# Kernel tuning notes

Hardware: AMD Instinct MI355X
Metric: run time of the kernel (lower is better)

Reference implementation:

```python
import jax, jax.numpy as jnp
import numpy as np

B, C_IN, C_OUT, H, W, K = 8, 64, 64, 64, 64, 9
T = H * W  # 4096 tokens
EPS = 1e-12  # F.normalize eps


def setup_inputs() -> dict:
    key = jax.random.key(0)
    ks = jax.random.split(key, 7)
    x = jax.random.normal(ks[0], (B, C_IN, H, W), dtype=jnp.float32)
    Wq = jax.random.normal(ks[1], (T, T), dtype=jnp.float32) * 0.02
    Wk = jax.random.normal(ks[2], (T, T), dtype=jnp.float32) * 0.02
    Wv = jax.random.normal(ks[3], (T, T), dtype=jnp.float32) * 0.02
    Wo = jax.random.normal(ks[4], (T, T), dtype=jnp.float32) * 0.02
    conv_w = jax.random.normal(ks[5], (C_OUT, C_IN, K), dtype=jnp.float32) * 0.05
    conv_b = jax.random.normal(ks[6], (C_OUT,), dtype=jnp.float32) * 0.01
    return {"x": x, "Wq": Wq, "Wk": Wk, "Wv": Wv, "Wo": Wo,
            "conv_w": conv_w, "conv_b": conv_b}


def reference(x, Wq, Wk, Wv, Wo, conv_w, conv_b):
    Bq, Cc, Hh, Ww = x.shape
    Tt = Hh * Ww
    xf = x.reshape(Bq, Cc, Tt)  # flatten(start_dim=2)
    # nn.Linear over the token (last) dim: y[...,s] = sum_t x[...,t] * W[s,t]
    q = jnp.einsum('bct,st->bcs', xf, Wq)
    k = jnp.einsum('bct,st->bcs', xf, Wk)
    v = jnp.einsum('bct,st->bcs', xf, Wv)
    # cosine similarity over channel dim (dim=1), clamp to >= 0
    kn = k / jnp.maximum(jnp.linalg.norm(k, axis=1, keepdims=True), EPS)
    qn = q / jnp.maximum(jnp.linalg.norm(q, axis=1, keepdims=True), EPS)
    sim = jnp.clip(jnp.einsum('bct,bcs->bts', kn, qn), 0.0, None)  # [B,T,T]
    # top-K most similar neighbors per token (largest=True for similarity)
    _, idx = jax.lax.top_k(sim, K)  # [B,T,K] int32
    # gather neighbor values: prime[b,c,t,j] = v[b,c,idx[b,t,j]]
    gather = jax.vmap(lambda vv, ii: vv[:, ii])  # vv:[C,T], ii:[T,K] -> [C,T,K]
    prime = gather(v, idx).reshape(Bq, Cc, Tt * K)
    # Conv1d(kernel=K, stride=K, padding=0): aggregates each K-neighbor group
    out = jax.lax.conv_general_dilated(
        prime, conv_w, window_strides=(K,), padding='VALID',
        dimension_numbers=('NCH', 'OIH', 'NCH'))  # [B,C_OUT,T]
    out = out + conv_b[None, :, None]
    out = jnp.einsum('bct,st->bcs', out, Wo)  # w_o over token dim
    return out.reshape(Bq, conv_w.shape[0], Hh, Ww)
```

## Files before the change

kernel.cpp:

```cpp
#include <hip/hip_runtime.h>

#define T4096 4096
#define CH 64
typedef unsigned long long u64;

__global__ __launch_bounds__(512) void gemm_qkv(
    const float* __restrict__ X,
    const float* __restrict__ Wq, const float* __restrict__ Wk, const float* __restrict__ Wv,
    float* __restrict__ QT, float* __restrict__ KT, float* __restrict__ VT)
{
    const float* W = (blockIdx.z == 0) ? Wq : (blockIdx.z == 1) ? Wk : Wv;
    float*       O = (blockIdx.z == 0) ? QT : (blockIdx.z == 1) ? KT : VT;
    const int b  = blockIdx.y;
    const int s0 = blockIdx.x * 128;

    __shared__ float As[64][132];
    __shared__ float Bs[64][68];

    const int tid = threadIdx.x;
    const int tx = tid & 15;   const int c0 = tx * 4;
    const int my = tid >> 4;   const int m0 = my * 4;
    const int lr = tid >> 3;
    const int lk = (tid & 7) * 4;
    const int sw = lk;

    float acc[4][4];
#pragma unroll
    for (int i = 0; i < 4; ++i)
#pragma unroll
        for (int j = 0; j < 4; ++j) acc[i][j] = 0.f;

    const float* Xb = X + (size_t)b * CH * T4096;

    for (int k0 = 0; k0 < T4096; k0 += 64) {
#pragma unroll
        for (int kk = 0; kk < 2; ++kk) {
            const int kb = 32 * kk + lk;
#pragma unroll
            for (int p = 0; p < 2; ++p) {
                int row = lr + 64 * p;
                float4 v = *(const float4*)(W + (size_t)(s0 + row) * T4096 + k0 + kb);
                int col = row ^ sw;
                As[kb + 0][col] = v.x; As[kb + 1][col] = v.y;
                As[kb + 2][col] = v.z; As[kb + 3][col] = v.w;
            }
            {
                int row = lr;
                float4 v = *(const float4*)(Xb + (size_t)row * T4096 + k0 + kb);
                int col = row ^ sw;
                Bs[kb + 0][col] = v.x; Bs[kb + 1][col] = v.y;
                Bs[kb + 2][col] = v.z; Bs[kb + 3][col] = v.w;
            }
        }
        __syncthreads();
#pragma unroll
        for (int k = 0; k < 64; ++k) {
            const int swk = k & 28;
            float4 a  = *(const float4*)&As[k][m0 ^ swk];
            float4 bv = *(const float4*)&Bs[k][c0 ^ swk];
            float am[4] = {a.x, a.y, a.z, a.w};
            float bn[4] = {bv.x, bv.y, bv.z, bv.w};
#pragma unroll
            for (int i = 0; i < 4; ++i)
#pragma unroll
                for (int j = 0; j < 4; ++j) acc[i][j] = fmaf(am[i], bn[j], acc[i][j]);
        }
        __syncthreads();
    }
    if (blockIdx.z == 0) {
#pragma unroll
        for (int i = 0; i < 4; ++i) {
            int s = s0 + m0 + i;
            *(float4*)(O + ((((size_t)b * 64 + (s >> 6)) * 16 + tx) * 64 + (s & 63)) * 4) =
                make_float4(acc[i][0], acc[i][1], acc[i][2], acc[i][3]);
        }
    } else {
#pragma unroll
        for (int i = 0; i < 4; ++i) {
            *(float4*)(O + ((size_t)b * T4096 + s0 + m0 + i) * CH + c0) =
                make_float4(acc[i][0], acc[i][1], acc[i][2], acc[i][3]);
        }
    }
}

__global__ __launch_bounds__(256) void normalize_qk(float* __restrict__ QT, float* __restrict__ KT)
{
    int gtok = blockIdx.x * 4 + (threadIdx.x >> 6);
    int lane = threadIdx.x & 63;
    bool isQ = (gtok < 8 * T4096);
    int t = gtok & (T4096 - 1);
    int b = (gtok >> 12) & 7;
    float* p;
    if (isQ) p = QT + ((((size_t)b * 64 + (t >> 6)) * 16 + (lane >> 2)) * 64 + (t & 63)) * 4 + (lane & 3);
    else     p = KT + ((size_t)b * T4096 + t) * CH + lane;
    float v = *p;
    float ss = v * v;
#pragma unroll
    for (int off = 32; off; off >>= 1) ss += __shfl_xor(ss, off);
    float n = fmaxf(sqrtf(ss), 1e-12f);
    *p = v / n;
}

__global__ __launch_bounds__(512) void sim_topk(
    const float* __restrict__ Qr, const float* __restrict__ KT, int* __restrict__ IDX)
{
    const int wg = blockIdx.x;
    const int b  = wg & 7;
    const int t0 = (wg >> 3) * 32;

    __shared__ float Kn[32][68];

    const int tid = threadIdx.x;
    const int tx = tid & 31;
    const int ty = tid >> 5;

    {
        int row = tid >> 4; int cc = (tid & 15) * 4;
        *(float4*)&Kn[row][cc] =
            *(const float4*)(KT + ((size_t)b * T4096 + t0 + row) * CH + cc);
    }
    __syncthreads();

    u64 tv[2][9];
#pragma unroll
    for (int r = 0; r < 2; ++r)
#pragma unroll
        for (int q = 0; q < 9; ++q) tv[r][q] = 0ULL;
    u64 thr[2] = {0ULL, 0ULL};
    unsigned thr_hi[2] = {0u, 0u};

    const float* qb0 = Qr + ((size_t)b * 64 * 1024 + tx) * 4;

    for (int it = 0; it < 16; ++it) {
        const float* bp = qb0 + (size_t)(it * 4) * 4096;
        float acc[2][8];
#pragma unroll
        for (int c = 0; c < 8; ++c) { acc[0][c] = 0.f; acc[1][c] = 0.f; }

#pragma unroll 1
        for (int c4g = 0; c4g < 16; ++c4g) {
            float4 qv[8];
#pragma unroll
            for (int cc = 0; cc < 8; ++cc)
                qv[cc] = *(const float4*)(bp + (size_t)(cc >> 1) * 4096
                                             + c4g * 256 + (cc & 1) * 128);
            float4 k0 = *(const float4*)&Kn[ty][c4g * 4];
            float4 k1 = *(const float4*)&Kn[16 + ty][c4g * 4];
#pragma unroll
            for (int cc = 0; cc < 8; ++cc) {
                acc[0][cc] = fmaf(k0.x, qv[cc].x, acc[0][cc]);
                acc[0][cc] = fmaf(k0.y, qv[cc].y, acc[0][cc]);
                acc[0][cc] = fmaf(k0.z, qv[cc].z, acc[0][cc]);
                acc[0][cc] = fmaf(k0.w, qv[cc].w, acc[0][cc]);
                acc[1][cc] = fmaf(k1.x, qv[cc].x, acc[1][cc]);
                acc[1][cc] = fmaf(k1.y, qv[cc].y, acc[1][cc]);
                acc[1][cc] = fmaf(k1.z, qv[cc].z, acc[1][cc]);
                acc[1][cc] = fmaf(k1.w, qv[cc].w, acc[1][cc]);
            }
        }

        bool ins = false;
        const int sb = it * 256 + tx;
#pragma unroll
        for (int rr = 0; rr < 2; ++rr)
#pragma unroll
            for (int cc = 0; cc < 8; ++cc) {
                float v = fmaxf(acc[rr][cc], 0.f);
                unsigned vb = __float_as_uint(v);
                if (vb >= thr_hi[rr]) {
                    int s = sb + 32 * cc;
                    u64 key = ((u64)vb << 32) | (u64)(4095 - s);
                    if (key > thr[rr]) {
                        u64 cv = key;
#pragma unroll
                        for (int p = 0; p < 9; ++p) {
                            u64 t  = tv[rr][p];
                            bool g = cv > t;
                            tv[rr][p] = g ? cv : t;
                            cv        = g ? t  : cv;
                        }
                        ins = true;
                    }
                }
            }
        if (__any(ins)) {
#pragma unroll
            for (int r = 0; r < 2; ++r) {
                u64 m = tv[r][8];
#pragma unroll
                for (int msk = 1; msk < 32; msk <<= 1) {
                    u64 o = __shfl_xor(m, msk);
                    if (o > m) m = o;
                }
                thr[r] = m;
                thr_hi[r] = (unsigned)(m >> 32);
            }
        }
    }

#pragma unroll
    for (int rr = 0; rr < 2; ++rr) {
        u64 mv[9];
#pragma unroll
        for (int q = 0; q < 9; ++q) mv[q] = tv[rr][q];
        const int outrow = t0 + rr * 16 + ty;
        int* dst = IDX + ((size_t)b * T4096 + outrow) * 9;
        for (int sel = 0; sel < 9; ++sel) {
            u64 bk = mv[0]; int bl = tx;
#pragma unroll
            for (int m = 1; m < 32; m <<= 1) {
                u64 ok = __shfl_xor(bk, m);
                int ol = __shfl_xor(bl, m);
                if (ok > bk) { bk = ok; bl = ol; }
            }
            if (tx == 0) dst[sel] = 4095 - (int)(unsigned)bk;
            if (tx == bl) {
#pragma unroll
                for (int q = 0; q < 8; ++q) mv[q] = mv[q + 1];
                mv[8] = 0ULL;
            }
        }
    }
}

__global__ void transpose_w(const float* __restrict__ cw, float* __restrict__ wT3)
{
    int idx = blockIdx.x * 256 + threadIdx.x;
    if (idx >= 64 * 64 * 9) return;
    int q   = idx & 3;
    int o   = (idx >> 2) & 63;
    int i4g = (idx >> 8) & 15;
    int j   = idx >> 12;
    wT3[idx] = cw[o * 576 + (i4g * 4 + q) * 9 + j];
}

__global__ __launch_bounds__(256) void gather_conv(
    const float* __restrict__ VT, const int* __restrict__ IDX,
    const float* __restrict__ wT3, const float* __restrict__ conv_b,
    float* __restrict__ out1)
{
    const int b  = blockIdx.y;
    const int w  = threadIdx.x >> 6;
    const int o  = threadIdx.x & 63;
    const int t0 = (blockIdx.x * 4 + w) * 4;

    __shared__ float vv[4][4][9][64];
    __shared__ int   nb[4][36];

    if (o < 36) nb[w][o] = IDX[((size_t)b * T4096 + t0) * 9 + o];
    __syncthreads();

#pragma unroll
    for (int tok = 0; tok < 4; ++tok)
#pragma unroll
        for (int j = 0; j < 9; ++j) {
            int n = nb[w][tok * 9 + j];
            vv[w][tok][j][o] = VT[((size_t)b * T4096 + n) * CH + o];
        }
    __syncthreads();

    float cb = conv_b[o];
    float a0 = cb, a1 = cb, a2 = cb, a3 = cb;
    for (int j = 0; j < 9; ++j) {
#pragma unroll
        for (int i4 = 0; i4 < 16; ++i4) {
            float4 w4 = *(const float4*)(wT3 + (((size_t)j * 16 + i4) * 64 + o) * 4);
            float4 v0 = *(const float4*)&vv[w][0][j][i4 * 4];
            float4 v1 = *(const float4*)&vv[w][1][j][i4 * 4];
            float4 v2 = *(const float4*)&vv[w][2][j][i4 * 4];
            float4 v3 = *(const float4*)&vv[w][3][j][i4 * 4];
            a0 = fmaf(v0.x, w4.x, a0); a0 = fmaf(v0.y, w4.y, a0); a0 = fmaf(v0.z, w4.z, a0); a0 = fmaf(v0.w, w4.w, a0);
            a1 = fmaf(v1.x, w4.x, a1); a1 = fmaf(v1.y, w4.y, a1); a1 = fmaf(v1.z, w4.z, a1); a1 = fmaf(v1.w, w4.w, a1);
            a2 = fmaf(v2.x, w4.x, a2); a2 = fmaf(v2.y, w4.y, a2); a2 = fmaf(v2.z, w4.z, a2); a2 = fmaf(v2.w, w4.w, a2);
            a3 = fmaf(v3.x, w4.x, a3); a3 = fmaf(v3.y, w4.y, a3); a3 = fmaf(v3.z, w4.z, a3); a3 = fmaf(v3.w, w4.w, a3);
        }
    }
    out1[((size_t)b * T4096 + t0 + 0) * CH + o] = a0;
    out1[((size_t)b * T4096 + t0 + 1) * CH + o] = a1;
    out1[((size_t)b * T4096 + t0 + 2) * CH + o] = a2;
    out1[((size_t)b * T4096 + t0 + 3) * CH + o] = a3;
}

__global__ __launch_bounds__(256) void gemm_out(
    const float* __restrict__ out1, const float* __restrict__ Wo, float* __restrict__ Out)
{
    const int b  = blockIdx.y;
    const int s0 = blockIdx.x * 64;
    __shared__ float As[64][68];
    __shared__ float Bs[64][68];
    const int tid = threadIdx.x;
    const int tx = tid & 15;  const int sl = tx * 4;
    const int my = tid >> 4;  const int c0 = my * 4;
    const int lk = (tid & 7) * 4;
    const int sw = lk;

    float acc[4][4];
#pragma unroll
    for (int i = 0; i < 4; ++i)
#pragma unroll
        for (int j = 0; j < 4; ++j) acc[i][j] = 0.f;

    for (int k0 = 0; k0 < T4096; k0 += 64) {
        {
            int r  = tid >> 2;
            int cL = (tid & 3) * 16;
            const float* src = out1 + ((size_t)b * T4096 + k0 + r) * CH + cL;
#pragma unroll
            for (int q = 0; q < 4; ++q)
                *(float4*)&As[r][cL + 4 * q] = *(const float4*)(src + 4 * q);
        }
#pragma unroll
        for (int kk = 0; kk < 2; ++kk) {
            const int kb = 32 * kk + lk;
#pragma unroll
            for (int p = 0; p < 2; ++p) {
                int row = (tid >> 3) + 32 * p;
                float4 v = *(const float4*)(Wo + (size_t)(s0 + row) * T4096 + k0 + kb);
                int col = row ^ sw;
                Bs[kb + 0][col] = v.x; Bs[kb + 1][col] = v.y;
                Bs[kb + 2][col] = v.z; Bs[kb + 3][col] = v.w;
            }
        }
        __syncthreads();
#pragma unroll
        for (int k = 0; k < 64; ++k) {
            const int swk = k & 28;
            float4 a  = *(const float4*)&As[k][c0];
            float4 bv = *(const float4*)&Bs[k][sl ^ swk];
            float av[4] = {a.x, a.y, a.z, a.w};
            float bn[4] = {bv.x, bv.y, bv.z, bv.w};
#pragma unroll
            for (int i = 0; i < 4; ++i)
#pragma unroll
                for (int j = 0; j < 4; ++j) acc[i][j] = fmaf(av[i], bn[j], acc[i][j]);
        }
        __syncthreads();
    }
#pragma unroll
    for (int i = 0; i < 4; ++i) {
        float* dst = Out + ((size_t)b * CH + c0 + i) * T4096 + s0 + sl;
        *(float4*)dst = make_float4(acc[i][0], acc[i][1], acc[i][2], acc[i][3]);
    }
}

extern "C" void kernel_launch(void* const* d_in, const int* in_sizes, int n_in,
                              void* d_out, int out_size, void* d_ws, size_t ws_size,
                              hipStream_t stream)
{
    const float* x  = (const float*)d_in[0];
    const float* Wq = (const float*)d_in[1];
    const float* Wk = (const float*)d_in[2];
    const float* Wv = (const float*)d_in[3];
    const float* Wo = (const float*)d_in[4];
    const float* cw = (const float*)d_in[5];
    const float* cb = (const float*)d_in[6];
    float* Out = (float*)d_out;

    char* ws = (char*)d_ws;
    float* QT   = (float*)(ws);
    float* KT   = (float*)(ws + (size_t)8  * 1024 * 1024);
    float* VT   = (float*)(ws + (size_t)16 * 1024 * 1024);
    int*   IDXb = (int*)  (ws + (size_t)24 * 1024 * 1024);
    float* wT3  = (float*)(ws + (size_t)26 * 1024 * 1024);
    float* out1 = QT;

    gemm_qkv<<<dim3(32, 8, 3), dim3(512), 0, stream>>>(x, Wq, Wk, Wv, QT, KT, VT);
    normalize_qk<<<dim3(16384), dim3(256), 0, stream>>>(QT, KT);
    sim_topk<<<dim3(1024), dim3(512), 0, stream>>>(QT, KT, IDXb);
    transpose_w<<<dim3(144), dim3(256), 0, stream>>>(cw, wT3);
    gather_conv<<<dim3(256, 8), dim3(256), 0, stream>>>(VT, IDXb, wT3, cb, out1);
    gemm_out<<<dim3(64, 8), dim3(256), 0, stream>>>(out1, Wo, Out);
}
```

Before: 1.618 ms.

## Restructure sim_topk to one row per thread with split-S partial top-k merge

```diff
diff --git a/kernel.cpp b/kernel.cpp
--- a/kernel.cpp
+++ b/kernel.cpp
@@ -67,19 +67,10 @@
         }
         __syncthreads();
     }
-    if (blockIdx.z == 0) {
-#pragma unroll
-        for (int i = 0; i < 4; ++i) {
-            int s = s0 + m0 + i;
-            *(float4*)(O + ((((size_t)b * 64 + (s >> 6)) * 16 + tx) * 64 + (s & 63)) * 4) =
-                make_float4(acc[i][0], acc[i][1], acc[i][2], acc[i][3]);
-        }
-    } else {
-#pragma unroll
-        for (int i = 0; i < 4; ++i) {
-            *(float4*)(O + ((size_t)b * T4096 + s0 + m0 + i) * CH + c0) =
-                make_float4(acc[i][0], acc[i][1], acc[i][2], acc[i][3]);
-        }
+#pragma unroll
+    for (int i = 0; i < 4; ++i) {
+        *(float4*)(O + ((size_t)b * T4096 + s0 + m0 + i) * CH + c0) =
+            make_float4(acc[i][0], acc[i][1], acc[i][2], acc[i][3]);
     }
 }
 
@@ -87,12 +78,9 @@
 {
     int gtok = blockIdx.x * 4 + (threadIdx.x >> 6);
     int lane = threadIdx.x & 63;
-    bool isQ = (gtok < 8 * T4096);
-    int t = gtok & (T4096 - 1);
-    int b = (gtok >> 12) & 7;
-    float* p;
-    if (isQ) p = QT + ((((size_t)b * 64 + (t >> 6)) * 16 + (lane >> 2)) * 64 + (t & 63)) * 4 + (lane & 3);
-    else     p = KT + ((size_t)b * T4096 + t) * CH + lane;
+    float* base = (gtok < 8 * T4096) ? QT : KT;
+    int t = gtok & (8 * T4096 - 1);
+    float* p = base + (size_t)t * CH + lane;
     float v = *p;
     float ss = v * v;
 #pragma unroll
@@ -101,126 +89,111 @@
     *p = v / n;
 }
 
-__global__ __launch_bounds__(512) void sim_topk(
-    const float* __restrict__ Qr, const float* __restrict__ KT, int* __restrict__ IDX)
+__global__ __launch_bounds__(256, 2) void sim_topk(
+    const float* __restrict__ QT, const float* __restrict__ KT,
+    unsigned* __restrict__ PKv, unsigned short* __restrict__ PKi)
 {
     const int wg = blockIdx.x;
     const int b  = wg & 7;
-    const int t0 = (wg >> 3) * 32;
-
-    __shared__ float Kn[32][68];
-
-    const int tid = threadIdx.x;
-    const int tx = tid & 31;
-    const int ty = tid >> 5;
-
-    {
-        int row = tid >> 4; int cc = (tid & 15) * 4;
-        *(float4*)&Kn[row][cc] =
-            *(const float4*)(KT + ((size_t)b * T4096 + t0 + row) * CH + cc);
-    }
-    __syncthreads();
-
-    u64 tv[2][9];
-#pragma unroll
-    for (int r = 0; r < 2; ++r)
-#pragma unroll
-        for (int q = 0; q < 9; ++q) tv[r][q] = 0ULL;
-    u64 thr[2] = {0ULL, 0ULL};
-    unsigned thr_hi[2] = {0u, 0u};
-
-    const float* qb0 = Qr + ((size_t)b * 64 * 1024 + tx) * 4;
-
-    for (int it = 0; it < 16; ++it) {
-        const float* bp = qb0 + (size_t)(it * 4) * 4096;
-        float acc[2][8];
-#pragma unroll
-        for (int c = 0; c < 8; ++c) { acc[0][c] = 0.f; acc[1][c] = 0.f; }
+    const int sp = (wg >> 3) & 3;
+    const int rt = wg >> 5;
+    const int row = rt * 256 + threadIdx.x;
+
+    float4 kr[16];
+    const float* kp = KT + ((size_t)b * T4096 + row) * CH;
+#pragma unroll
+    for (int i = 0; i < 16; ++i) kr[i] = *(const float4*)(kp + 4 * i);
+
+    u64 tv[9];
+#pragma unroll
+    for (int q = 0; q < 9; ++q) tv[q] = 0ULL;
+    unsigned thr_hi = 0u;
+
+    const float* qb = QT + ((size_t)b * T4096 + sp * 1024) * CH;
 
 #pragma unroll 1
-        for (int c4g = 0; c4g < 16; ++c4g) {
-            float4 qv[8];
-#pragma unroll
-            for (int cc = 0; cc < 8; ++cc)
-                qv[cc] = *(const float4*)(bp + (size_t)(cc >> 1) * 4096
-                                             + c4g * 256 + (cc & 1) * 128);
-            float4 k0 = *(const float4*)&Kn[ty][c4g * 4];
-            float4 k1 = *(const float4*)&Kn[16 + ty][c4g * 4];
-#pragma unroll
-            for (int cc = 0; cc < 8; ++cc) {
-                acc[0][cc] = fmaf(k0.x, qv[cc].x, acc[0][cc]);
-                acc[0][cc] = fmaf(k0.y, qv[cc].y, acc[0][cc]);
-                acc[0][cc] = fmaf(k0.z, qv[cc].z, acc[0][cc]);
-                acc[0][cc] = fmaf(k0.w, qv[cc].w, acc[0][cc]);
-                acc[1][cc] = fmaf(k1.x, qv[cc].x, acc[1][cc]);
-                acc[1][cc] = fmaf(k1.y, qv[cc].y, acc[1][cc]);
-                acc[1][cc] = fmaf(k1.z, qv[cc].z, acc[1][cc]);
-                acc[1][cc] = fmaf(k1.w, qv[cc].w, acc[1][cc]);
-            }
-        }
-
-        bool ins = false;
-        const int sb = it * 256 + tx;
-#pragma unroll
-        for (int rr = 0; rr < 2; ++rr)
-#pragma unroll
-            for (int cc = 0; cc < 8; ++cc) {
-                float v = fmaxf(acc[rr][cc], 0.f);
-                unsigned vb = __float_as_uint(v);
-                if (vb >= thr_hi[rr]) {
-                    int s = sb + 32 * cc;
-                    u64 key = ((u64)vb << 32) | (u64)(4095 - s);
-                    if (key > thr[rr]) {
-                        u64 cv = key;
-#pragma unroll
-                        for (int p = 0; p < 9; ++p) {
-                            u64 t  = tv[rr][p];
-                            bool g = cv > t;
-                            tv[rr][p] = g ? cv : t;
-                            cv        = g ? t  : cv;
-                        }
-                        ins = true;
+    for (int qs = 0; qs < 256; ++qs) {
+        const float* base = qb + (size_t)qs * (4 * CH);
+        float a0 = 0.f, a1 = 0.f, a2 = 0.f, a3 = 0.f;
+#pragma unroll
+        for (int c = 0; c < 16; ++c) {
+            float4 q0 = *(const float4*)(base + c * 4);
+            float4 q1 = *(const float4*)(base + CH + c * 4);
+            float4 q2 = *(const float4*)(base + 2 * CH + c * 4);
+            float4 q3 = *(const float4*)(base + 3 * CH + c * 4);
+            a0 = fmaf(kr[c].x, q0.x, a0); a0 = fmaf(kr[c].y, q0.y, a0);
+            a0 = fmaf(kr[c].z, q0.z, a0); a0 = fmaf(kr[c].w, q0.w, a0);
+            a1 = fmaf(kr[c].x, q1.x, a1); a1 = fmaf(kr[c].y, q1.y, a1);
+            a1 = fmaf(kr[c].z, q1.z, a1); a1 = fmaf(kr[c].w, q1.w, a1);
+            a2 = fmaf(kr[c].x, q2.x, a2); a2 = fmaf(kr[c].y, q2.y, a2);
+            a2 = fmaf(kr[c].z, q2.z, a2); a2 = fmaf(kr[c].w, q2.w, a2);
+            a3 = fmaf(kr[c].x, q3.x, a3); a3 = fmaf(kr[c].y, q3.y, a3);
+            a3 = fmaf(kr[c].z, q3.z, a3); a3 = fmaf(kr[c].w, q3.w, a3);
+        }
+        const int s0 = sp * 1024 + qs * 4;
+        float av[4] = {a0, a1, a2, a3};
+#pragma unroll
+        for (int j = 0; j < 4; ++j) {
+            float v = fmaxf(av[j], 0.f);
+            unsigned vb = __float_as_uint(v);
+            if (vb >= thr_hi) {
+                u64 key = ((u64)vb << 32) | (u64)(4095 - (s0 + j));
+                if (key > tv[8]) {
+                    u64 cv = key;
+#pragma unroll
+                    for (int p = 0; p < 9; ++p) {
+                        u64 t  = tv[p];
+                        bool g = cv > t;
+                        tv[p] = g ? cv : t;
+                        cv    = g ? t  : cv;
                     }
+                    thr_hi = (unsigned)(tv[8] >> 32);
                 }
             }
-        if (__any(ins)) {
-#pragma unroll
-            for (int r = 0; r < 2; ++r) {
-                u64 m = tv[r][8];
-#pragma unroll
-                for (int msk = 1; msk < 32; msk <<= 1) {
-                    u64 o = __shfl_xor(m, msk);
-                    if (o > m) m = o;
-                }
-                thr[r] = m;
-                thr_hi[r] = (unsigned)(m >> 32);
-            }
-        }
-    }
-
-#pragma unroll
-    for (int rr = 0; rr < 2; ++rr) {
-        u64 mv[9];
-#pragma unroll
-        for (int q = 0; q < 9; ++q) mv[q] = tv[rr][q];
-        const int outrow = t0 + rr * 16 + ty;
-        int* dst = IDX + ((size_t)b * T4096 + outrow) * 9;
-        for (int sel = 0; sel < 9; ++sel) {
-            u64 bk = mv[0]; int bl = tx;
-#pragma unroll
-            for (int m = 1; m < 32; m <<= 1) {
-                u64 ok = __shfl_xor(bk, m);
-                int ol = __shfl_xor(bl, m);
-                if (ok > bk) { bk = ok; bl = ol; }
-            }
-            if (tx == 0) dst[sel] = 4095 - (int)(unsigned)bk;
-            if (tx == bl) {
-#pragma unroll
-                for (int q = 0; q < 8; ++q) mv[q] = mv[q + 1];
-                mv[8] = 0ULL;
-            }
-        }
-    }
+        }
+    }
+
+    const size_t o = (((size_t)b * 4 + sp) * T4096 + row) * 9;
+#pragma unroll
+    for (int q = 0; q < 9; ++q) {
+        PKv[o + q] = (unsigned)(tv[q] >> 32);
+        PKi[o + q] = (unsigned short)(tv[q] & 0xffffULL);
+    }
+}
+
+__global__ __launch_bounds__(256) void topk_merge(
+    const unsigned* __restrict__ PKv, const unsigned short* __restrict__ PKi,
+    int* __restrict__ IDX)
+{
+    const int t = blockIdx.x * 256 + threadIdx.x;
+    const int b = t >> 12;
+    const int row = t & 4095;
+
+    u64 tv[9];
+#pragma unroll
+    for (int q = 0; q < 9; ++q) tv[q] = 0ULL;
+
+    for (int sp = 0; sp < 4; ++sp) {
+        const size_t o = (((size_t)b * 4 + sp) * T4096 + row) * 9;
+#pragma unroll 1
+        for (int q = 0; q < 9; ++q) {
+            u64 key = ((u64)PKv[o + q] << 32) | (u64)PKi[o + q];
+            if (key <= tv[8]) break;
+            u64 cv = key;
+#pragma unroll
+            for (int p = 0; p < 9; ++p) {
+                u64 tt = tv[p];
+                bool g = cv > tt;
+                tv[p] = g ? cv : tt;
+                cv    = g ? tt : cv;
+            }
+        }
+    }
+
+    int* dst = IDX + ((size_t)b * T4096 + row) * 9;
+#pragma unroll
+    for (int q = 0; q < 9; ++q)
+        dst[q] = 4095 - (int)(unsigned)(tv[q] & 0xffffULL);
 }
 
 __global__ void transpose_w(const float* __restrict__ cw, float* __restrict__ wT3)
@@ -364,9 +337,13 @@
     float* wT3  = (float*)(ws + (size_t)26 * 1024 * 1024);
     float* out1 = QT;
 
+    unsigned*       PKv = (unsigned*)d_out;
+    unsigned short* PKi = (unsigned short*)((char*)d_out + (size_t)5 * 1024 * 1024);
+
     gemm_qkv<<<dim3(32, 8, 3), dim3(512), 0, stream>>>(x, Wq, Wk, Wv, QT, KT, VT);
     normalize_qk<<<dim3(16384), dim3(256), 0, stream>>>(QT, KT);
-    sim_topk<<<dim3(1024), dim3(512), 0, stream>>>(QT, KT, IDXb);
+    sim_topk<<<dim3(512), dim3(256), 0, stream>>>(QT, KT, PKv, PKi);
+    topk_merge<<<dim3(128), dim3(256), 0, stream>>>(PKv, PKi, IDXb);
     transpose_w<<<dim3(144), dim3(256), 0, stream>>>(cw, wT3);
     gather_conv<<<dim3(256, 8), dim3(256), 0, stream>>>(VT, IDXb, wT3, cb, out1);
     gemm_out<<<dim3(64, 8), dim3(256), 0, stream>>>(out1, Wo, Out);
```

Result: slower. 1.870 ms (+15.6%).

## Stage Q tiles in shared memory and use 4x4 register tiling in sim_topk

Applied to the files above, without the earlier changes.

```diff
diff --git a/kernel.cpp b/kernel.cpp
--- a/kernel.cpp
+++ b/kernel.cpp
@@ -101,83 +101,100 @@
     *p = v / n;
 }
 
-__global__ __launch_bounds__(512) void sim_topk(
+__global__ __launch_bounds__(512, 2) void sim_topk(
     const float* __restrict__ Qr, const float* __restrict__ KT, int* __restrict__ IDX)
 {
     const int wg = blockIdx.x;
     const int b  = wg & 7;
-    const int t0 = (wg >> 3) * 32;
-
-    __shared__ float Kn[32][68];
-
-    const int tid = threadIdx.x;
-    const int tx = tid & 31;
-    const int ty = tid >> 5;
+    const int r0 = (wg >> 3) * 64;
+
+    __shared__ float Kn[64][68];
+    __shared__ float Qs[64][132];
+
+    const int tid  = threadIdx.x;
+    const int colg = tid & 31;
+    const int rowg = tid >> 5;
 
     {
-        int row = tid >> 4; int cc = (tid & 15) * 4;
-        *(float4*)&Kn[row][cc] =
-            *(const float4*)(KT + ((size_t)b * T4096 + t0 + row) * CH + cc);
-    }
-    __syncthreads();
-
-    u64 tv[2][9];
-#pragma unroll
-    for (int r = 0; r < 2; ++r)
+        int row = tid >> 3;
+        int c8  = (tid & 7) * 8;
+        const float* src = KT + ((size_t)b * T4096 + r0 + row) * CH + c8;
+        float4 v0 = *(const float4*)(src);
+        float4 v1 = *(const float4*)(src + 4);
+        int rp = row ^ ((tid & 7) << 3);
+        Kn[c8 + 0][rp] = v0.x; Kn[c8 + 1][rp] = v0.y;
+        Kn[c8 + 2][rp] = v0.z; Kn[c8 + 3][rp] = v0.w;
+        Kn[c8 + 4][rp] = v1.x; Kn[c8 + 5][rp] = v1.y;
+        Kn[c8 + 6][rp] = v1.z; Kn[c8 + 7][rp] = v1.w;
+    }
+
+    u64 tv[4][9];
+#pragma unroll
+    for (int r = 0; r < 4; ++r)
 #pragma unroll
         for (int q = 0; q < 9; ++q) tv[r][q] = 0ULL;
-    u64 thr[2] = {0ULL, 0ULL};
-    unsigned thr_hi[2] = {0u, 0u};
-
-    const float* qb0 = Qr + ((size_t)b * 64 * 1024 + tx) * 4;
-
-    for (int it = 0; it < 16; ++it) {
-        const float* bp = qb0 + (size_t)(it * 4) * 4096;
-        float acc[2][8];
-#pragma unroll
-        for (int c = 0; c < 8; ++c) { acc[0][c] = 0.f; acc[1][c] = 0.f; }
-
-#pragma unroll 1
-        for (int c4g = 0; c4g < 16; ++c4g) {
-            float4 qv[8];
-#pragma unroll
-            for (int cc = 0; cc < 8; ++cc)
-                qv[cc] = *(const float4*)(bp + (size_t)(cc >> 1) * 4096
-                                             + c4g * 256 + (cc & 1) * 128);
-            float4 k0 = *(const float4*)&Kn[ty][c4g * 4];
-            float4 k1 = *(const float4*)&Kn[16 + ty][c4g * 4];
-#pragma unroll
-            for (int cc = 0; cc < 8; ++cc) {
-                acc[0][cc] = fmaf(k0.x, qv[cc].x, acc[0][cc]);
-                acc[0][cc] = fmaf(k0.y, qv[cc].y, acc[0][cc]);
-                acc[0][cc] = fmaf(k0.z, qv[cc].z, acc[0][cc]);
-                acc[0][cc] = fmaf(k0.w, qv[cc].w, acc[0][cc]);
-                acc[1][cc] = fmaf(k1.x, qv[cc].x, acc[1][cc]);
-                acc[1][cc] = fmaf(k1.y, qv[cc].y, acc[1][cc]);
-                acc[1][cc] = fmaf(k1.z, qv[cc].z, acc[1][cc]);
-                acc[1][cc] = fmaf(k1.w, qv[cc].w, acc[1][cc]);
-            }
+    u64 thr[4] = {0ULL, 0ULL, 0ULL, 0ULL};
+    unsigned thr_hi[4] = {0u, 0u, 0u, 0u};
+
+    for (int chk = 0; chk < 32; ++chk) {
+        const int c0 = chk * 128;
+        __syncthreads();
+        {
+            int col  = tid >> 2;
+            int cQ   = (tid & 3) * 16;
+            int gcol = c0 + col;
+            const float* qb = Qr + ((((size_t)b * 64 + (gcol >> 6)) * 16 + (cQ >> 2)) * 64
+                                    + (gcol & 63)) * 4;
+            int cp = col ^ ((cQ >> 4) << 3);
+#pragma unroll
+            for (int i = 0; i < 4; ++i) {
+                float4 v = *(const float4*)(qb + (size_t)i * 256);
+                int c = cQ + i * 4;
+                Qs[c + 0][cp] = v.x; Qs[c + 1][cp] = v.y;
+                Qs[c + 2][cp] = v.z; Qs[c + 3][cp] = v.w;
+            }
+        }
+        __syncthreads();
+
+        float acc[4][4];
+#pragma unroll
+        for (int i = 0; i < 4; ++i)
+#pragma unroll
+            for (int j = 0; j < 4; ++j) acc[i][j] = 0.f;
+
+#pragma unroll 8
+        for (int c = 0; c < 64; ++c) {
+            const int g8 = ((c >> 3) & 7) << 3;
+            const int g4 = ((c >> 4) & 3) << 3;
+            float4 kv = *(const float4*)&Kn[c][(rowg * 4) ^ g8];
+            float4 qv = *(const float4*)&Qs[c][(colg * 4) ^ g4];
+            float km[4] = {kv.x, kv.y, kv.z, kv.w};
+            float qm[4] = {qv.x, qv.y, qv.z, qv.w};
+#pragma unroll
+            for (int i = 0; i < 4; ++i)
+#pragma unroll
+                for (int j = 0; j < 4; ++j)
+                    acc[i][j] = fmaf(km[i], qm[j], acc[i][j]);
         }
 
         bool ins = false;
-        const int sb = it * 256 + tx;
-#pragma unroll
-        for (int rr = 0; rr < 2; ++rr)
-#pragma unroll
-            for (int cc = 0; cc < 8; ++cc) {
-                float v = fmaxf(acc[rr][cc], 0.f);
+#pragma unroll
+        for (int i = 0; i < 4; ++i)
+#pragma unroll
+            for (int j = 0; j < 4; ++j) {
+                float v = fmaxf(acc[i][j], 0.f);
                 unsigned vb = __float_as_uint(v);
-                if (vb >= thr_hi[rr]) {
-                    int s = sb + 32 * cc;
+                if (vb >= thr_hi[i]) {
+                    int s = c0 + colg * 4 + j;
                     u64 key = ((u64)vb << 32) | (u64)(4095 - s);
-                    if (key > thr[rr]) {
+                    if (key > thr[i]) {
                         u64 cv = key;
 #pragma unroll
                         for (int p = 0; p < 9; ++p) {
-                            u64 t  = tv[rr][p];
+                            u64 t  = tv[i][p];
                             bool g = cv > t;
-                            tv[rr][p] = g ? cv : t;
-                            cv        = g ? t  : cv;
+                            tv[i][p] = g ? cv : t;
+                            cv       = g ? t  : cv;
                         }
                         ins = true;
                     }
@@ -185,7 +202,7 @@
             }
         if (__any(ins)) {
 #pragma unroll
-            for (int r = 0; r < 2; ++r) {
+            for (int r = 0; r < 4; ++r) {
                 u64 m = tv[r][8];
 #pragma unroll
                 for (int msk = 1; msk < 32; msk <<= 1) {
@@ -199,22 +216,22 @@
     }
 
 #pragma unroll
-    for (int rr = 0; rr < 2; ++rr) {
+    for (int i = 0; i < 4; ++i) {
         u64 mv[9];
 #pragma unroll
-        for (int q = 0; q < 9; ++q) mv[q] = tv[rr][q];
-        const int outrow = t0 + rr * 16 + ty;
+        for (int q = 0; q < 9; ++q) mv[q] = tv[i][q];
+        const int outrow = r0 + rowg * 4 + i;
         int* dst = IDX + ((size_t)b * T4096 + outrow) * 9;
         for (int sel = 0; sel < 9; ++sel) {
-            u64 bk = mv[0]; int bl = tx;
+            u64 bk = mv[0]; int bl = colg;
 #pragma unroll
             for (int m = 1; m < 32; m <<= 1) {
                 u64 ok = __shfl_xor(bk, m);
                 int ol = __shfl_xor(bl, m);
                 if (ok > bk) { bk = ok; bl = ol; }
             }
-            if (tx == 0) dst[sel] = 4095 - (int)(unsigned)bk;
-            if (tx == bl) {
+            if (colg == 0) dst[sel] = 4095 - (int)(unsigned)(bk & 0xffffULL);
+            if (colg == bl) {
 #pragma unroll
                 for (int q = 0; q < 8; ++q) mv[q] = mv[q + 1];
                 mv[8] = 0ULL;
@@ -366,7 +383,7 @@
 
     gemm_qkv<<<dim3(32, 8, 3), dim3(512), 0, stream>>>(x, Wq, Wk, Wv, QT, KT, VT);
     normalize_qk<<<dim3(16384), dim3(256), 0, stream>>>(QT, KT);
-    sim_topk<<<dim3(1024), dim3(512), 0, stream>>>(QT, KT, IDXb);
+    sim_topk<<<dim3(512), dim3(512), 0, stream>>>(QT, KT, IDXb);
     transpose_w<<<dim3(144), dim3(256), 0, stream>>>(cw, wT3);
     gather_conv<<<dim3(256, 8), dim3(256), 0, stream>>>(VT, IDXb, wT3, cb, out1);
     gemm_out<<<dim3(64, 8), dim3(256), 0, stream>>>(out1, Wo, Out);
```

Result: slower. 1.703 ms (+5.3%).

## Fuse Q/K normalization into QKV GEMM epilogue and enlarge per-thread tiles

Applied to the files above, without the earlier changes.

```diff
diff --git a/kernel.cpp b/kernel.cpp
--- a/kernel.cpp
+++ b/kernel.cpp
@@ -3,14 +3,14 @@
 #define T4096 4096
 #define CH 64
 typedef unsigned long long u64;
-
-__global__ __launch_bounds__(512) void gemm_qkv(
+typedef float v2f __attribute__((ext_vector_type(2)));
+
+__global__ __launch_bounds__(128) void gemm_qkv(
     const float* __restrict__ X,
     const float* __restrict__ Wq, const float* __restrict__ Wk, const float* __restrict__ Wv,
     float* __restrict__ QT, float* __restrict__ KT, float* __restrict__ VT)
 {
     const float* W = (blockIdx.z == 0) ? Wq : (blockIdx.z == 1) ? Wk : Wv;
-    float*       O = (blockIdx.z == 0) ? QT : (blockIdx.z == 1) ? KT : VT;
     const int b  = blockIdx.y;
     const int s0 = blockIdx.x * 128;
 
@@ -18,87 +18,100 @@
     __shared__ float Bs[64][68];
 
     const int tid = threadIdx.x;
-    const int tx = tid & 15;   const int c0 = tx * 4;
-    const int my = tid >> 4;   const int m0 = my * 4;
-    const int lr = tid >> 3;
-    const int lk = (tid & 7) * 4;
-    const int sw = lk;
-
-    float acc[4][4];
-#pragma unroll
-    for (int i = 0; i < 4; ++i)
-#pragma unroll
-        for (int j = 0; j < 4; ++j) acc[i][j] = 0.f;
+    const int txc = tid & 7;   const int c0 = txc * 8;
+    const int tym = tid >> 3;  const int m0 = tym * 8;
+    const int lk  = (tid & 15) * 4;
+    const int rA  = tid >> 4;
+    const int sw  = lk & 28;
+
+    float acc[8][8];
+#pragma unroll
+    for (int i = 0; i < 8; ++i)
+#pragma unroll
+        for (int j = 0; j < 8; ++j) acc[i][j] = 0.f;
 
     const float* Xb = X + (size_t)b * CH * T4096;
 
     for (int k0 = 0; k0 < T4096; k0 += 64) {
-#pragma unroll
-        for (int kk = 0; kk < 2; ++kk) {
-            const int kb = 32 * kk + lk;
-#pragma unroll
-            for (int p = 0; p < 2; ++p) {
-                int row = lr + 64 * p;
-                float4 v = *(const float4*)(W + (size_t)(s0 + row) * T4096 + k0 + kb);
-                int col = row ^ sw;
-                As[kb + 0][col] = v.x; As[kb + 1][col] = v.y;
-                As[kb + 2][col] = v.z; As[kb + 3][col] = v.w;
-            }
-            {
-                int row = lr;
-                float4 v = *(const float4*)(Xb + (size_t)row * T4096 + k0 + kb);
-                int col = row ^ sw;
-                Bs[kb + 0][col] = v.x; Bs[kb + 1][col] = v.y;
-                Bs[kb + 2][col] = v.z; Bs[kb + 3][col] = v.w;
-            }
+#pragma unroll 4
+        for (int p = 0; p < 16; ++p) {
+            int row = rA + 8 * p;
+            float4 v = *(const float4*)(W + (size_t)(s0 + row) * T4096 + k0 + lk);
+            int col = row ^ sw;
+            As[lk + 0][col] = v.x; As[lk + 1][col] = v.y;
+            As[lk + 2][col] = v.z; As[lk + 3][col] = v.w;
+        }
+#pragma unroll 4
+        for (int p = 0; p < 8; ++p) {
+            int row = rA + 8 * p;
+            float4 v = *(const float4*)(Xb + (size_t)row * T4096 + k0 + lk);
+            int col = row ^ sw;
+            Bs[lk + 0][col] = v.x; Bs[lk + 1][col] = v.y;
+            Bs[lk + 2][col] = v.z; Bs[lk + 3][col] = v.w;
         }
         __syncthreads();
 #pragma unroll
         for (int k = 0; k < 64; ++k) {
             const int swk = k & 28;
-            float4 a  = *(const float4*)&As[k][m0 ^ swk];
-            float4 bv = *(const float4*)&Bs[k][c0 ^ swk];
-            float am[4] = {a.x, a.y, a.z, a.w};
-            float bn[4] = {bv.x, bv.y, bv.z, bv.w};
-#pragma unroll
-            for (int i = 0; i < 4; ++i)
-#pragma unroll
-                for (int j = 0; j < 4; ++j) acc[i][j] = fmaf(am[i], bn[j], acc[i][j]);
+            float4 a0 = *(const float4*)&As[k][(m0) ^ swk];
+            float4 a1 = *(const float4*)&As[k][(m0 + 4) ^ swk];
+            float4 b0 = *(const float4*)&Bs[k][(c0) ^ swk];
+            float4 b1 = *(const float4*)&Bs[k][(c0 + 4) ^ swk];
+            float am[8] = {a0.x,a0.y,a0.z,a0.w,a1.x,a1.y,a1.z,a1.w};
+            float bn[8] = {b0.x,b0.y,b0.z,b0.w,b1.x,b1.y,b1.z,b1.w};
+#pragma unroll
+            for (int i = 0; i < 8; ++i)
+#pragma unroll
+                for (int j = 0; j < 8; ++j)
+                    acc[i][j] = fmaf(am[i], bn[j], acc[i][j]);
         }
         __syncthreads();
     }
-    if (blockIdx.z == 0) {
-#pragma unroll
-        for (int i = 0; i < 4; ++i) {
+
+    if (blockIdx.z == 2) {
+#pragma unroll
+        for (int i = 0; i < 8; ++i) {
             int s = s0 + m0 + i;
-            *(float4*)(O + ((((size_t)b * 64 + (s >> 6)) * 16 + tx) * 64 + (s & 63)) * 4) =
-                make_float4(acc[i][0], acc[i][1], acc[i][2], acc[i][3]);
-        }
-    } else {
-#pragma unroll
-        for (int i = 0; i < 4; ++i) {
-            *(float4*)(O + ((size_t)b * T4096 + s0 + m0 + i) * CH + c0) =
-                make_float4(acc[i][0], acc[i][1], acc[i][2], acc[i][3]);
-        }
-    }
-}
-
-__global__ __launch_bounds__(256) void normalize_qk(float* __restrict__ QT, float* __restrict__ KT)
-{
-    int gtok = blockIdx.x * 4 + (threadIdx.x >> 6);
-    int lane = threadIdx.x & 63;
-    bool isQ = (gtok < 8 * T4096);
-    int t = gtok & (T4096 - 1);
-    int b = (gtok >> 12) & 7;
-    float* p;
-    if (isQ) p = QT + ((((size_t)b * 64 + (t >> 6)) * 16 + (lane >> 2)) * 64 + (t & 63)) * 4 + (lane & 3);
-    else     p = KT + ((size_t)b * T4096 + t) * CH + lane;
-    float v = *p;
-    float ss = v * v;
-#pragma unroll
-    for (int off = 32; off; off >>= 1) ss += __shfl_xor(ss, off);
-    float n = fmaxf(sqrtf(ss), 1e-12f);
-    *p = v / n;
+            float* dst = VT + ((size_t)b * T4096 + s) * CH + c0;
+            *(float4*)(dst)     = make_float4(acc[i][0], acc[i][1], acc[i][2], acc[i][3]);
+            *(float4*)(dst + 4) = make_float4(acc[i][4], acc[i][5], acc[i][6], acc[i][7]);
+        }
+        return;
+    }
+
+#pragma unroll
+    for (int i = 0; i < 8; ++i) {
+        float p[8];
+#pragma unroll
+        for (int j = 0; j < 8; ++j) p[j] = acc[i][j] * acc[i][j];
+#pragma unroll
+        for (int j = 0; j < 8; ++j) p[j] += __shfl_xor(p[j], 4);
+#pragma unroll
+        for (int j = 0; j < 8; ++j) p[j] += __shfl_xor(p[j], 2);
+#pragma unroll
+        for (int j = 0; j < 8; ++j) p[j] += __shfl_xor(p[j], 1);
+        float s4[8];
+#pragma unroll
+        for (int j = 0; j < 8; ++j) s4[j] = p[j] + p[j ^ 4];
+        float s2[8];
+#pragma unroll
+        for (int j = 0; j < 8; ++j) s2[j] = s4[j] + s4[j ^ 2];
+        float ss = s2[0] + s2[1];
+        float n  = fmaxf(sqrtf(ss), 1e-12f);
+
+        int s = s0 + m0 + i;
+        if (blockIdx.z == 0) {
+            size_t t0q = (((size_t)b * 64 + (s >> 6)) * 16 + (c0 >> 2)) * 64 + (s & 63);
+            *(float4*)(QT + t0q * 4) =
+                make_float4(acc[i][0] / n, acc[i][1] / n, acc[i][2] / n, acc[i][3] / n);
+            *(float4*)(QT + (t0q + 64) * 4) =
+                make_float4(acc[i][4] / n, acc[i][5] / n, acc[i][6] / n, acc[i][7] / n);
+        } else {
+            float* dst = KT + ((size_t)b * T4096 + s) * CH + c0;
+            *(float4*)(dst)     = make_float4(acc[i][0] / n, acc[i][1] / n, acc[i][2] / n, acc[i][3] / n);
+            *(float4*)(dst + 4) = make_float4(acc[i][4] / n, acc[i][5] / n, acc[i][6] / n, acc[i][7] / n);
+        }
+    }
 }
 
 __global__ __launch_bounds__(512) void sim_topk(
@@ -177,7 +190,7 @@
                             u64 t  = tv[rr][p];
                             bool g = cv > t;
                             tv[rr][p] = g ? cv : t;
-                            cv        = g ? t  : cv;
+                            cv       = g ? t  : cv;
                         }
                         ins = true;
                     }
@@ -213,7 +226,7 @@
                 int ol = __shfl_xor(bl, m);
                 if (ok > bk) { bk = ok; bl = ol; }
             }
-            if (tx == 0) dst[sel] = 4095 - (int)(unsigned)bk;
+            if (tx == 0) dst[sel] = 4095 - (int)(unsigned)(bk & 0xffffULL);
             if (tx == bl) {
 #pragma unroll
                 for (int q = 0; q < 8; ++q) mv[q] = mv[q + 1];
@@ -294,11 +307,9 @@
     const int lk = (tid & 7) * 4;
     const int sw = lk;
 
-    float acc[4][4];
-#pragma unroll
-    for (int i = 0; i < 4; ++i)
-#pragma unroll
-        for (int j = 0; j < 4; ++j) acc[i][j] = 0.f;
+    v2f acc2[4][2];
+#pragma unroll
+    for (int i = 0; i < 4; ++i) { acc2[i][0] = (v2f)0.f; acc2[i][1] = (v2f)0.f; }
 
     for (int k0 = 0; k0 < T4096; k0 += 64) {
         {
@@ -327,19 +338,22 @@
             const int swk = k & 28;
             float4 a  = *(const float4*)&As[k][c0];
             float4 bv = *(const float4*)&Bs[k][sl ^ swk];
+            v2f b0 = {bv.x, bv.y};
+            v2f b1 = {bv.z, bv.w};
             float av[4] = {a.x, a.y, a.z, a.w};
-            float bn[4] = {bv.x, bv.y, bv.z, bv.w};
-#pragma unroll
-            for (int i = 0; i < 4; ++i)
-#pragma unroll
-                for (int j = 0; j < 4; ++j) acc[i][j] = fmaf(av[i], bn[j], acc[i][j]);
+#pragma unroll
+            for (int i = 0; i < 4; ++i) {
+                v2f as = {av[i], av[i]};
+                acc2[i][0] = __builtin_elementwise_fma(as, b0, acc2[i][0]);
+                acc2[i][1] = __builtin_elementwise_fma(as, b1, acc2[i][1]);
+            }
         }
         __syncthreads();
     }
 #pragma unroll
     for (int i = 0; i < 4; ++i) {
         float* dst = Out + ((size_t)b * CH + c0 + i) * T4096 + s0 + sl;
-        *(float4*)dst = make_float4(acc[i][0], acc[i][1], acc[i][2], acc[i][3]);
+        *(float4*)dst = make_float4(acc2[i][0].x, acc2[i][0].y, acc2[i][1].x, acc2[i][1].y);
     }
 }
 
@@ -364,8 +378,7 @@
     float* wT3  = (float*)(ws + (size_t)26 * 1024 * 1024);
     float* out1 = QT;
 
-    gemm_qkv<<<dim3(32, 8, 3), dim3(512), 0, stream>>>(x, Wq, Wk, Wv, QT, KT, VT);
-    normalize_qk<<<dim3(16384), dim3(256), 0, stream>>>(QT, KT);
+    gemm_qkv<<<dim3(32, 8, 3), dim3(128), 0, stream>>>(x, Wq, Wk, Wv, QT, KT, VT);
     sim_topk<<<dim3(1024), dim3(512), 0, stream>>>(QT, KT, IDXb);
     transpose_w<<<dim3(144), dim3(256), 0, stream>>>(cw, wT3);
     gather_conv<<<dim3(256, 8), dim3(256), 0, stream>>>(VT, IDXb, wT3, cb, out1);
```

Measured after the change: 1.987 ms. +22.8%, slower.
